# Kernel tuning notes

Hardware: AMD Instinct MI355X
Metric: run time of the kernel (lower is better)

The kernel has to match this reference:

```python
import jax, jax.numpy as jnp
import numpy as np

N, C, H, O, NUM_CLASSES = 4096, 768, 512, 50, 1


def setup_inputs() -> dict:
    key = jax.random.key(0)
    ks = jax.random.split(key, 8)
    x = jax.random.normal(ks[0], (N, C), dtype=jnp.float32)
    labels = jax.random.randint(ks[1], (N,), 0, 2, dtype=jnp.int64)
    W1 = jax.random.normal(ks[2], (C, H), dtype=jnp.float32) / np.sqrt(C)
    b1 = jnp.zeros((H,), dtype=jnp.float32)
    W2 = jax.random.normal(ks[3], (H, O), dtype=jnp.float32) / np.sqrt(H)
    b2 = jnp.zeros((O,), dtype=jnp.float32)
    fcW = jax.random.normal(ks[4], (C + O, NUM_CLASSES), dtype=jnp.float32) / np.sqrt(C + O)
    fcb = jnp.zeros((NUM_CLASSES,), dtype=jnp.float32)
    return {"x": x, "labels": labels, "W1": W1, "b1": b1, "W2": W2, "b2": b2, "fcW": fcW, "fcb": fcb}


def _build_graph(x, labels):
    # similarity-threshold edge construction (dense masked form of the python double loop)
    sim = x @ x.T                                   # [N, N]
    n = x.shape[0]
    diff = labels[:, None] != labels[None, :]       # cross-label pairs
    cnt = jnp.sum(diff)
    s = jnp.sum(jnp.where(diff, sim, 0.0))
    threshold = jnp.where(cnt > 0, s / cnt.astype(sim.dtype), jnp.asarray(0.0, sim.dtype))
    eye = jnp.eye(n, dtype=bool)
    same = (labels[:, None] == labels[None, :]) & ~eye
    edge_mask = same & (sim <= threshold)           # symmetric (sim symmetric)
    loss_mask = edge_mask & (jnp.arange(n)[:, None] < jnp.arange(n)[None, :])  # i<j pairs
    adj = jax.lax.stop_gradient(edge_mask.astype(x.dtype))
    # GCN normalization with self-loops
    a = adj + jnp.eye(n, dtype=x.dtype)
    dinv = jax.lax.rsqrt(jnp.sum(a, axis=1))        # deg >= 1
    norm_adj = dinv[:, None] * a * dinv[None, :]
    return norm_adj, loss_mask


def reference(x, labels, W1, b1, W2, b2, fcW, fcb):
    norm_adj, loss_mask = _build_graph(x, labels)
    h = jax.nn.relu(norm_adj @ (x @ W1) + b1)       # conv1 + relu
    g = norm_adj @ (h @ W2) + b2                    # conv2
    f_g = jnp.concatenate([x, g], axis=-1)          # [N, C+O]
    out = f_g @ fcW + fcb                           # [N, 1]
    return out, f_g, loss_mask, x
```

## Files before the change

kernel.cpp:

```cpp
#include <hip/hip_runtime.h>
#include <hip/hip_bf16.h>
#include <math.h>

#define NN 4096
#define CD 768
#define HD 512
#define OD 50
#define FGD 818

typedef short short8 __attribute__((ext_vector_type(8)));
typedef _Float16 half8 __attribute__((ext_vector_type(8)));
typedef float f32x4 __attribute__((ext_vector_type(4)));
typedef unsigned short us4 __attribute__((ext_vector_type(4)));
typedef unsigned short ushortT;
typedef unsigned char uchar;
typedef unsigned long long u64;

__device__ inline ushortT f2bf(float v) {
    __hip_bfloat16 b = __float2bfloat16(v);
    return *(ushortT*)&b;
}
__device__ inline float bf2f(ushortT u) {
    __hip_bfloat16 b = *(__hip_bfloat16*)&u;
    return __bfloat162float(b);
}
__device__ inline float dinv_of(int d) {
    return (float)(1.0 / sqrt((double)(1 + d)));
}

__global__ __launch_bounds__(256) void gsum_kernel(const float* __restrict__ x,
                                                   const int* __restrict__ labels,
                                                   double* __restrict__ gsum) {
    int b = blockIdx.x;
    int t = threadIdx.x;
    double a0[3] = {0, 0, 0}, a1[3] = {0, 0, 0};
    for (int rr = 0; rr < 16; ++rr) {
        int row = b * 16 + rr;
        int lab = labels[row];
#pragma unroll
        for (int s = 0; s < 3; ++s) {
            double v = (double)x[(size_t)row * CD + t + s * 256];
            if (lab == 0) a0[s] += v; else a1[s] += v;
        }
    }
#pragma unroll
    for (int s = 0; s < 3; ++s) {
        atomicAdd(&gsum[t + s * 256], a0[s]);
        atomicAdd(&gsum[768 + t + s * 256], a1[s]);
    }
}

__global__ __launch_bounds__(256) void gdot_kernel(const double* __restrict__ gsum,
                                                   const int* __restrict__ labels,
                                                   double* __restrict__ scal) {
    int t = threadIdx.x;
    double d = 0.0;
    for (int c = t; c < CD; c += 256) d += gsum[c] * gsum[768 + c];
    int n0 = 0;
    for (int i = t; i < NN; i += 256) n0 += (labels[i] == 0) ? 1 : 0;
    for (int off = 32; off; off >>= 1) {
        d += __shfl_down(d, off);
        n0 += __shfl_down(n0, off);
    }
    __shared__ double sd[4];
    __shared__ int sn[4];
    int wid = t >> 6, lane = t & 63;
    if (lane == 0) { sd[wid] = d; sn[wid] = n0; }
    __syncthreads();
    if (t == 0) {
        double D = sd[0] + sd[1] + sd[2] + sd[3];
        double N0 = (double)(sn[0] + sn[1] + sn[2] + sn[3]);
        scal[0] = 2.0 * D;
        scal[1] = 2.0 * N0 * ((double)NN - N0);
    }
}

#define BAND 0.10
#define RC_CAP (1 << 18)
#define RCB 256

__global__ __launch_bounds__(256) void sim_fused(
    const ushortT* __restrict__ xf, const int* __restrict__ labels,
    const double* __restrict__ scal, u64* __restrict__ abbits,
    float* __restrict__ lm, int* __restrict__ deg,
    int* __restrict__ rc_cnt, int* __restrict__ rc_list) {
    int bid = blockIdx.x;
    int sid = (bid & 7) * 260 + (bid >> 3);
    int sby = 0, rem = sid;
    for (; sby < 8; ++sby) {
        int rowsz = 36 + (7 - sby) * 64;
        if (rem < rowsz) break;
        rem -= rowsz;
    }
    int sbx, iby, ibx;
    if (rem < 36) {
        sbx = sby;
        iby = 0;
        while (rem >= 8 - iby) { rem -= 8 - iby; ++iby; }
        ibx = iby + rem;
    } else {
        rem -= 36;
        sbx = sby + 1 + (rem >> 6);
        int u = rem & 63;
        iby = u >> 3; ibx = u & 7;
    }
    int by = sby * 8 + iby, bx = sbx * 8 + ibx;
    bool diag = (bx == by);

    __shared__ ushortT lds[2 * 64 * 72];
    __shared__ int larr[128];
    __shared__ int rcbuf[RCB];
    __shared__ int rcn, rcbase;
    int tid = threadIdx.x;
    int lane = tid & 63;
    int w = tid >> 6;
    int wr = w >> 1, wc = w & 1;
    int m = lane & 15, quad = lane >> 4;
    int row0 = by * 64, col0 = bx * 64;

    if (tid == 0) rcn = 0;
    if (tid < 64) larr[tid] = labels[row0 + tid];
    else if (tid < 128) larr[tid] = labels[col0 + tid - 64];

    f32x4 acc[2][2] = {{{0.f, 0.f, 0.f, 0.f}, {0.f, 0.f, 0.f, 0.f}},
                       {{0.f, 0.f, 0.f, 0.f}, {0.f, 0.f, 0.f, 0.f}}};

    const size_t rowbase = (size_t)row0 * CD;
    const size_t colbase = (size_t)col0 * CD;
    short8 rg[2][2];
#pragma unroll
    for (int tt = 0; tt < 2; ++tt) {
        int id2 = tid + tt * 256;
        int row = id2 >> 3, c8 = (id2 & 7) * 8;
        rg[tt][0] = *(const short8*)&xf[rowbase + (size_t)row * CD + c8];
        rg[tt][1] = *(const short8*)&xf[colbase + (size_t)row * CD + c8];
    }

    for (int k0 = 0; k0 < CD; k0 += 64) {
        __syncthreads();
#pragma unroll
        for (int tt = 0; tt < 2; ++tt) {
            int id2 = tid + tt * 256;
            int row = id2 >> 3, c8 = (id2 & 7) * 8;
            *(short8*)&lds[0 * 4608 + row * 72 + c8] = rg[tt][0];
            *(short8*)&lds[1 * 4608 + row * 72 + c8] = rg[tt][1];
        }
        __syncthreads();
        if (k0 + 64 < CD) {
#pragma unroll
            for (int tt = 0; tt < 2; ++tt) {
                int id2 = tid + tt * 256;
                int row = id2 >> 3, c8 = (id2 & 7) * 8 + k0 + 64;
                rg[tt][0] = *(const short8*)&xf[rowbase + (size_t)row * CD + c8];
                rg[tt][1] = *(const short8*)&xf[colbase + (size_t)row * CD + c8];
            }
        }
#pragma unroll
        for (int ks = 0; ks < 2; ++ks) {
            half8 ah[2], bh[2];
#pragma unroll
            for (int i = 0; i < 2; ++i)
                ah[i] = *(const half8*)&lds[(wr * 32 + i * 16 + m) * 72 +
                                            ks * 32 + quad * 8];
#pragma unroll
            for (int j = 0; j < 2; ++j)
                bh[j] = *(const half8*)&lds[4608 + (wc * 32 + j * 16 + m) * 72 +
                                            ks * 32 + quad * 8];
#pragma unroll
            for (int i = 0; i < 2; ++i)
#pragma unroll
                for (int j = 0; j < 2; ++j)
                    acc[i][j] = __builtin_amdgcn_mfma_f32_16x16x32_f16(
                        ah[i], bh[j], acc[i][j], 0, 0, 0);
        }
    }
    __syncthreads();

    double thrd;
    {
        double cnt = scal[1];
        thrd = (cnt > 0.0) ? (scal[0] / cnt) : 0.0;
    }
    uchar* flags = (uchar*)lds;
#pragma unroll
    for (int i = 0; i < 2; ++i)
#pragma unroll
        for (int j = 0; j < 2; ++j) {
#pragma unroll
            for (int r = 0; r < 4; ++r) {
                int row = wr * 32 + i * 16 + quad * 4 + r;
                int col = wc * 32 + j * 16 + m;
                bool same = (larr[row] == larr[64 + col]);
                bool selfp = ((row0 + row) == (col0 + col));
                bool edge = false;
                if (same && !selfp) {
                    double s = (double)acc[i][j][r];
                    if (s <= thrd - BAND) {
                        edge = true;
                    } else if (s <= thrd + BAND) {
                        edge = (s <= thrd);
                        int enc = ((row0 + row) << 12) | (col0 + col) |
                                  (diag ? 0 : (1 << 24)) |
                                  (edge ? (1 << 25) : 0);
                        int slot = atomicAdd(&rcn, 1);
                        if (slot < RCB) rcbuf[slot] = enc;
                    }
                }
                flags[row * 68 + col] = edge ? 1 : 0;
            }
        }
    __syncthreads();
    if (tid == 0) {
        int n = rcn < RCB ? rcn : RCB;
        rcbase = n ? atomicAdd(rc_cnt, n) : 0;
    }

    {
        int r = tid >> 2, q = tid & 3;
        int cnti = 0;
        unsigned int bits16 = 0;
#pragma unroll
        for (int s = 0; s < 4; ++s) {
            int cb = q * 16 + s * 4;
            float4 f;
#pragma unroll
            for (int k2 = 0; k2 < 4; ++k2) {
                int c = cb + k2;
                bool fl = flags[r * 68 + c] != 0;
                cnti += fl ? 1 : 0;
                if (fl || (diag && r == c)) bits16 |= 1u << (s * 4 + k2);
                ((float*)&f)[k2] = (fl && (row0 + r < col0 + c)) ? 1.0f : 0.0f;
            }
            *(float4*)&lm[(size_t)(row0 + r) * NN + col0 + cb] = f;
        }
        unsigned int s1 = __shfl_down(bits16, 1);
        unsigned int s2 = __shfl_down(bits16, 2);
        unsigned int s3 = __shfl_down(bits16, 3);
        cnti += __shfl_down(cnti, 1);
        cnti += __shfl_down(cnti, 2);
        if (q == 0) {
            u64 u = (u64)bits16 | ((u64)s1 << 16) | ((u64)s2 << 32) |
                    ((u64)s3 << 48);
            abbits[(size_t)(row0 + r) * 64 + bx] = u;
            if (cnti) atomicAdd(&deg[row0 + r], cnti);
        }
    }

    if (!diag) {
        int c = tid >> 2, q = tid & 3;
        int cnti = 0;
        unsigned int bits16 = 0;
        float4 fz = {0.0f, 0.0f, 0.0f, 0.0f};
#pragma unroll
        for (int s = 0; s < 4; ++s) {
            int rb = q * 16 + s * 4;
#pragma unroll
            for (int k2 = 0; k2 < 4; ++k2) {
                bool fl = flags[(rb + k2) * 68 + c] != 0;
                cnti += fl ? 1 : 0;
                if (fl) bits16 |= 1u << (s * 4 + k2);
            }
            *(float4*)&lm[(size_t)(col0 + c) * NN + row0 + rb] = fz;
        }
        unsigned int s1 = __shfl_down(bits16, 1);
        unsigned int s2 = __shfl_down(bits16, 2);
        unsigned int s3 = __shfl_down(bits16, 3);
        cnti += __shfl_down(cnti, 1);
        cnti += __shfl_down(cnti, 2);
        if (q == 0) {
            u64 u = (u64)bits16 | ((u64)s1 << 16) | ((u64)s2 << 32) |
                    ((u64)s3 << 48);
            abbits[(size_t)(col0 + c) * 64 + by] = u;
            if (cnti) atomicAdd(&deg[col0 + c], cnti);
        }
    }

    __syncthreads();
    {
        int n = rcn < RCB ? rcn : RCB;
        if (tid < n) {
            int idx = rcbase + tid;
            if (idx < RC_CAP) rc_list[idx] = rcbuf[tid];
        }
    }
}

__global__ __launch_bounds__(256) void rc_fix(
    const float* __restrict__ x, const double* __restrict__ scal,
    const int* __restrict__ rc_cnt, const int* __restrict__ rc_list,
    u64* __restrict__ abbits, float* __restrict__ lm, int* __restrict__ deg) {
    int cnt = *rc_cnt;
    if (cnt > RC_CAP) cnt = RC_CAP;
    double thrd;
    {
        double c = scal[1];
        thrd = (c > 0.0) ? (scal[0] / c) : 0.0;
    }
    int lane = threadIdx.x & 63;
    int wid = (blockIdx.x * 256 + threadIdx.x) >> 6;
    int nw = (gridDim.x * 256) >> 6;
    for (int e = wid; e < cnt; e += nw) {
        int enc = rc_list[e];
        int c = enc & 0xFFF;
        int r = (enc >> 12) & 0xFFF;
        bool mirror = (enc >> 24) & 1;
        bool prov = (enc >> 25) & 1;
        const float* xi = x + (size_t)r * CD;
        const float* xj = x + (size_t)c * CD;
        double d = 0.0;
#pragma unroll
        for (int s = 0; s < 12; ++s)
            d += (double)xi[lane + s * 64] * (double)xj[lane + s * 64];
        for (int off = 32; off; off >>= 1) d += __shfl_down(d, off);
        if (lane == 0) {
            bool exact = (d <= thrd);
            if (exact != prov) {
                u64 mk = 1ull << (c & 63);
                if (exact) atomicOr(&abbits[(size_t)r * 64 + (c >> 6)], mk);
                else       atomicAnd(&abbits[(size_t)r * 64 + (c >> 6)], ~mk);
                lm[(size_t)r * NN + c] = (exact && r < c) ? 1.0f : 0.0f;
                int dlt = exact ? 1 : -1;
                atomicAdd(&deg[r], dlt);
                if (mirror) {
                    u64 mk2 = 1ull << (r & 63);
                    if (exact) atomicOr(&abbits[(size_t)c * 64 + (r >> 6)], mk2);
                    else       atomicAnd(&abbits[(size_t)c * 64 + (r >> 6)], ~mk2);
                    atomicAdd(&deg[c], dlt);
                }
            }
        }
    }
}

__global__ __launch_bounds__(256) void prep_kernel(
    const float* __restrict__ x, const float* __restrict__ W1,
    const float* __restrict__ W2, float* __restrict__ fg, float* __restrict__ xo,
    ushortT* __restrict__ xh, ushortT* __restrict__ xf, ushortT* __restrict__ w1t,
    ushortT* __restrict__ w2t) {
    int b = blockIdx.x;
    if (b < 4096) {
        int t = threadIdx.x;
        if (t < 192) {
            float4 v = *(const float4*)&x[(size_t)b * CD + t * 4];
            *(float4*)&xo[(size_t)b * CD + t * 4] = v;
            fg[(size_t)b * FGD + t * 4 + 0] = v.x;
            fg[(size_t)b * FGD + t * 4 + 1] = v.y;
            fg[(size_t)b * FGD + t * 4 + 2] = v.z;
            fg[(size_t)b * FGD + t * 4 + 3] = v.w;
            us4 hh, ff;
            float* vp = (float*)&v;
#pragma unroll
            for (int k = 0; k < 4; ++k) {
                ((ushortT*)&hh)[k] = f2bf(vp[k]);
                _Float16 g = (_Float16)vp[k];
                ((ushortT*)&ff)[k] = *(ushortT*)&g;
            }
            *(us4*)&xh[(size_t)b * CD + t * 4] = hh;
            *(us4*)&xf[(size_t)b * CD + t * 4] = ff;
        }
        return;
    }
    __shared__ float tT[32][33];
    const float* P;
    ushortT* T;
    int K, N, Npad, k0, n0;
    if (b < 4480) {
        int bb = b - 4096;
        P = W1; T = w1t; K = CD; N = HD; Npad = HD;
        k0 = (bb % 24) * 32; n0 = (bb / 24) * 32;
    } else {
        int bb = b - 4480;
        P = W2; T = w2t; K = HD; N = OD; Npad = 64;
        k0 = (bb % 16) * 32; n0 = (bb / 16) * 32;
    }
    int tx = threadIdx.x & 31, ty = threadIdx.x >> 5;
#pragma unroll
    for (int s = 0; s < 4; ++s) {
        int k = k0 + ty + s * 8, n = n0 + tx;
        tT[ty + s * 8][tx] = (k < K && n < N) ? P[(size_t)k * N + n] : 0.0f;
    }
    __syncthreads();
#pragma unroll
    for (int s = 0; s < 4; ++s) {
        int n = n0 + ty + s * 8, k = k0 + tx;
        if (n < Npad && k < K) T[(size_t)n * K + k] = f2bf(tT[tx][ty + s * 8]);
    }
}

template <bool RELU, bool HASBIAS, int EPI>
__global__ __launch_bounds__(256) void gemm_bf16(
    const ushortT* __restrict__ A, const ushortT* __restrict__ B,
    ushortT* __restrict__ Cb, int M, int Nn, int K, int ldc,
    const int* __restrict__ deg, const float* __restrict__ bias) {
    __shared__ ushortT lds[2 * 64 * 72];
    int tid = threadIdx.x;
    int lane = tid & 63;
    int w = tid >> 6;
    int wr = w >> 1, wc = w & 1;
    int m = lane & 15, quad = lane >> 4;
    int row0 = blockIdx.y * 64, col0 = blockIdx.x * 64;

    f32x4 acc[2][2] = {{{0.f, 0.f, 0.f, 0.f}, {0.f, 0.f, 0.f, 0.f}},
                       {{0.f, 0.f, 0.f, 0.f}, {0.f, 0.f, 0.f, 0.f}}};

    for (int k0 = 0; k0 < K; k0 += 64) {
#pragma unroll
        for (int t = 0; t < 2; ++t) {
            int id2 = tid + t * 256;
            int row = id2 >> 3, c8 = (id2 & 7) * 8;
            *(short8*)&lds[row * 72 + c8] =
                *(const short8*)&A[(size_t)(row0 + row) * K + k0 + c8];
            *(short8*)&lds[4608 + row * 72 + c8] =
                *(const short8*)&B[(size_t)(col0 + row) * K + k0 + c8];
        }
        __syncthreads();
#pragma unroll
        for (int ks = 0; ks < 2; ++ks) {
            short8 af[2], bf[2];
#pragma unroll
            for (int i = 0; i < 2; ++i)
                af[i] = *(const short8*)&lds[(wr * 32 + i * 16 + m) * 72 +
                                             ks * 32 + quad * 8];
#pragma unroll
            for (int j = 0; j < 2; ++j)
                bf[j] = *(const short8*)&lds[4608 + (wc * 32 + j * 16 + m) * 72 +
                                             ks * 32 + quad * 8];
#pragma unroll
            for (int i = 0; i < 2; ++i)
#pragma unroll
                for (int j = 0; j < 2; ++j)
                    acc[i][j] = __builtin_amdgcn_mfma_f32_16x16x32_bf16(
                        af[i], bf[j], acc[i][j], 0, 0, 0);
        }
        __syncthreads();
    }

    if (EPI == 2) {
        ushortT* Th = lds;
#pragma unroll
        for (int i = 0; i < 2; ++i)
#pragma unroll
            for (int j = 0; j < 2; ++j)
#pragma unroll
                for (int r = 0; r < 4; ++r) {
                    int row = wr * 32 + i * 16 + quad * 4 + r;
                    int col = wc * 32 + j * 16 + m;
                    float dv = dinv_of(deg[row0 + row]);
                    Th[col * 72 + row] = f2bf(acc[i][j][r] * dv);
                }
        __syncthreads();
#pragma unroll
        for (int t = 0; t < 2; ++t) {
            int id2 = tid + t * 256;
            int cc = id2 >> 3, chunk = id2 & 7;
            *(short8*)&Cb[(size_t)(col0 + cc) * M + row0 + chunk * 8] =
                *(const short8*)&Th[cc * 72 + chunk * 8];
        }
    } else {
#pragma unroll
        for (int i = 0; i < 2; ++i)
#pragma unroll
            for (int j = 0; j < 2; ++j)
#pragma unroll
                for (int r = 0; r < 4; ++r) {
                    int row = wr * 32 + i * 16 + quad * 4 + r;
                    int col = wc * 32 + j * 16 + m;
                    int gr = row0 + row, gc = col0 + col;
                    if (gc < Nn) {
                        float v = acc[i][j][r] * dinv_of(deg[gr]);
                        if (HASBIAS) v += bias[gc];
                        if (RELU) v = fmaxf(v, 0.0f);
                        Cb[(size_t)gr * ldc + gc] = f2bf(v);
                    }
                }
    }
}

__global__ __launch_bounds__(256) void gemm_part(
    const ushortT* __restrict__ A, const ushortT* __restrict__ B,
    float* __restrict__ P, int M, int K, int KC) {
    __shared__ ushortT lds[2 * 64 * 72];
    int tid = threadIdx.x;
    int lane = tid & 63;
    int w = tid >> 6;
    int wr = w >> 1, wc = w & 1;
    int m = lane & 15, quad = lane >> 4;
    int kb = blockIdx.x;
    int row0 = blockIdx.y * 64;
    int kbase = kb * KC;

    f32x4 acc[2][2] = {{{0.f, 0.f, 0.f, 0.f}, {0.f, 0.f, 0.f, 0.f}},
                       {{0.f, 0.f, 0.f, 0.f}, {0.f, 0.f, 0.f, 0.f}}};

    for (int k0 = 0; k0 < KC; k0 += 64) {
#pragma unroll
        for (int t = 0; t < 2; ++t) {
            int id2 = tid + t * 256;
            int row = id2 >> 3, c8 = (id2 & 7) * 8;
            *(short8*)&lds[row * 72 + c8] =
                *(const short8*)&A[(size_t)(row0 + row) * K + kbase + k0 + c8];
            *(short8*)&lds[4608 + row * 72 + c8] =
                *(const short8*)&B[(size_t)row * K + kbase + k0 + c8];
        }
        __syncthreads();
#pragma unroll
        for (int ks = 0; ks < 2; ++ks) {
            short8 af[2], bf[2];
#pragma unroll
            for (int i = 0; i < 2; ++i)
                af[i] = *(const short8*)&lds[(wr * 32 + i * 16 + m) * 72 +
                                             ks * 32 + quad * 8];
#pragma unroll
            for (int j = 0; j < 2; ++j)
                bf[j] = *(const short8*)&lds[4608 + (wc * 32 + j * 16 + m) * 72 +
                                             ks * 32 + quad * 8];
#pragma unroll
            for (int i = 0; i < 2; ++i)
#pragma unroll
                for (int j = 0; j < 2; ++j)
                    acc[i][j] = __builtin_amdgcn_mfma_f32_16x16x32_bf16(
                        af[i], bf[j], acc[i][j], 0, 0, 0);
        }
        __syncthreads();
    }
#pragma unroll
    for (int i = 0; i < 2; ++i)
#pragma unroll
        for (int j = 0; j < 2; ++j)
#pragma unroll
            for (int r = 0; r < 4; ++r) {
                int row = wr * 32 + i * 16 + quad * 4 + r;
                int col = wc * 32 + j * 16 + m;
                P[((size_t)kb * M + row0 + row) * 64 + col] = acc[i][j][r];
            }
}

__global__ __launch_bounds__(256) void gemm_partB(
    const u64* __restrict__ Abits, const ushortT* __restrict__ B,
    float* __restrict__ P, int M, int K, int KC) {
    __shared__ ushortT lds[2 * 64 * 72];
    int tid = threadIdx.x;
    int lane = tid & 63;
    int w = tid >> 6;
    int wr = w >> 1, wc = w & 1;
    int m = lane & 15, quad = lane >> 4;
    int kb = blockIdx.x;
    int row0 = blockIdx.y * 64;
    int kbase = kb * KC;
    int er = tid >> 2, eq = tid & 3;

    f32x4 acc[2][2] = {{{0.f, 0.f, 0.f, 0.f}, {0.f, 0.f, 0.f, 0.f}},
                       {{0.f, 0.f, 0.f, 0.f}, {0.f, 0.f, 0.f, 0.f}}};

    for (int k0 = 0; k0 < KC; k0 += 64) {
#pragma unroll
        for (int t = 0; t < 2; ++t) {
            int id2 = tid + t * 256;
            int row = id2 >> 3, c8 = (id2 & 7) * 8;
            *(short8*)&lds[4608 + row * 72 + c8] =
                *(const short8*)&B[(size_t)row * K + kbase + k0 + c8];
        }
        {
            u64 bits = Abits[(size_t)(row0 + er) * 64 + ((kbase + k0) >> 6)];
            unsigned int half = (unsigned int)(bits >> (eq * 16)) & 0xFFFFu;
            short8 v0, v1;
#pragma unroll
            for (int k = 0; k < 8; ++k) {
                ((ushortT*)&v0)[k] =
                    ((half >> k) & 1) ? (ushortT)0x3F80 : (ushortT)0;
                ((ushortT*)&v1)[k] =
                    ((half >> (k + 8)) & 1) ? (ushortT)0x3F80 : (ushortT)0;
            }
            *(short8*)&lds[er * 72 + eq * 16] = v0;
            *(short8*)&lds[er * 72 + eq * 16 + 8] = v1;
        }
        __syncthreads();
#pragma unroll
        for (int ks = 0; ks < 2; ++ks) {
            short8 af[2], bf[2];
#pragma unroll
            for (int i = 0; i < 2; ++i)
                af[i] = *(const short8*)&lds[(wr * 32 + i * 16 + m) * 72 +
                                             ks * 32 + quad * 8];
#pragma unroll
            for (int j = 0; j < 2; ++j)
                bf[j] = *(const short8*)&lds[4608 + (wc * 32 + j * 16 + m) * 72 +
                                             ks * 32 + quad * 8];
#pragma unroll
            for (int i = 0; i < 2; ++i)
#pragma unroll
                for (int j = 0; j < 2; ++j)
                    acc[i][j] = __builtin_amdgcn_mfma_f32_16x16x32_bf16(
                        af[i], bf[j], acc[i][j], 0, 0, 0);
        }
        __syncthreads();
    }
#pragma unroll
    for (int i = 0; i < 2; ++i)
#pragma unroll
        for (int j = 0; j < 2; ++j)
#pragma unroll
            for (int r = 0; r < 4; ++r) {
                int row = wr * 32 + i * 16 + quad * 4 + r;
                int col = wc * 32 + j * 16 + m;
                P[((size_t)kb * M + row0 + row) * 64 + col] = acc[i][j][r];
            }
}

__global__ __launch_bounds__(256) void gemm_partWB(
    const u64* __restrict__ Abits, const ushortT* __restrict__ B,
    float* __restrict__ P, int M, int K, int KC, int ldP) {
    __shared__ ushortT lds[2 * 64 * 72];
    int tid = threadIdx.x;
    int lane = tid & 63;
    int w = tid >> 6;
    int wr = w >> 1, wc = w & 1;
    int m = lane & 15, quad = lane >> 4;
    int col0 = blockIdx.x * 64;
    int row0 = blockIdx.y * 64;
    int kb = blockIdx.z;
    int kbase = kb * KC;
    int er = tid >> 2, eq = tid & 3;

    f32x4 acc[2][2] = {{{0.f, 0.f, 0.f, 0.f}, {0.f, 0.f, 0.f, 0.f}},
                       {{0.f, 0.f, 0.f, 0.f}, {0.f, 0.f, 0.f, 0.f}}};

    for (int k0 = 0; k0 < KC; k0 += 64) {
#pragma unroll
        for (int t = 0; t < 2; ++t) {
            int id2 = tid + t * 256;
            int row = id2 >> 3, c8 = (id2 & 7) * 8;
            *(short8*)&lds[4608 + row * 72 + c8] =
                *(const short8*)&B[(size_t)(col0 + row) * K + kbase + k0 + c8];
        }
        {
            u64 bits = Abits[(size_t)(row0 + er) * 64 + ((kbase + k0) >> 6)];
            unsigned int half = (unsigned int)(bits >> (eq * 16)) & 0xFFFFu;
            short8 v0, v1;
#pragma unroll
            for (int k = 0; k < 8; ++k) {
                ((ushortT*)&v0)[k] =
                    ((half >> k) & 1) ? (ushortT)0x3F80 : (ushortT)0;
                ((ushortT*)&v1)[k] =
                    ((half >> (k + 8)) & 1) ? (ushortT)0x3F80 : (ushortT)0;
            }
            *(short8*)&lds[er * 72 + eq * 16] = v0;
            *(short8*)&lds[er * 72 + eq * 16 + 8] = v1;
        }
        __syncthreads();
#pragma unroll
        for (int ks = 0; ks < 2; ++ks) {
            short8 af[2], bf[2];
#pragma unroll
            for (int i = 0; i < 2; ++i)
                af[i] = *(const short8*)&lds[(wr * 32 + i * 16 + m) * 72 +
                                             ks * 32 + quad * 8];
#pragma unroll
            for (int j = 0; j < 2; ++j)
                bf[j] = *(const short8*)&lds[4608 + (wc * 32 + j * 16 + m) * 72 +
                                             ks * 32 + quad * 8];
#pragma unroll
            for (int i = 0; i < 2; ++i)
#pragma unroll
                for (int j = 0; j < 2; ++j)
                    acc[i][j] = __builtin_amdgcn_mfma_f32_16x16x32_bf16(
                        af[i], bf[j], acc[i][j], 0, 0, 0);
        }
        __syncthreads();
    }
#pragma unroll
    for (int i = 0; i < 2; ++i)
#pragma unroll
        for (int j = 0; j < 2; ++j)
#pragma unroll
            for (int r = 0; r < 4; ++r) {
                int row = wr * 32 + i * 16 + quad * 4 + r;
                int col = wc * 32 + j * 16 + m;
                P[((size_t)kb * M + row0 + row) * ldP + col0 + col] =
                    acc[i][j][r];
            }
}

__global__ __launch_bounds__(256) void k5_epi(const float* __restrict__ P5,
                                              const int* __restrict__ deg,
                                              const float* __restrict__ b1,
                                              ushortT* __restrict__ hb) {
    int tid = threadIdx.x;
    int cg = tid & 127;
    int rr = tid >> 7;
#pragma unroll
    for (int p = 0; p < 2; ++p) {
        int r = blockIdx.x * 4 + p * 2 + rr;
        float dv = dinv_of(deg[r]);
        float4 s = {0.f, 0.f, 0.f, 0.f};
#pragma unroll
        for (int kb = 0; kb < 4; ++kb) {
            float4 v = *(const float4*)&P5[((size_t)kb * NN + r) * HD + cg * 4];
            s.x += v.x; s.y += v.y; s.z += v.z; s.w += v.w;
        }
        float4 bv = *(const float4*)&b1[cg * 4];
        us4 o;
        o[0] = f2bf(fmaxf(s.x * dv + bv.x, 0.f));
        o[1] = f2bf(fmaxf(s.y * dv + bv.y, 0.f));
        o[2] = f2bf(fmaxf(s.z * dv + bv.z, 0.f));
        o[3] = f2bf(fmaxf(s.w * dv + bv.w, 0.f));
        *(us4*)&hb[(size_t)r * HD + cg * 4] = o;
    }
}

__global__ __launch_bounds__(256) void k6_epi(const float* __restrict__ P6,
                                              const int* __restrict__ deg,
                                              ushortT* __restrict__ hw2sT) {
    __shared__ ushortT Th[64 * 72];
    int row0 = blockIdx.x * 64;
    int tid = threadIdx.x;
    int rl = tid >> 2, q = tid & 3;
    float dv = dinv_of(deg[row0 + rl]);
#pragma unroll
    for (int s = 0; s < 16; ++s) {
        int c = q * 16 + s;
        float v = 0.f;
#pragma unroll
        for (int kb = 0; kb < 8; ++kb)
            v += P6[((size_t)kb * NN + row0 + rl) * 64 + c];
        Th[c * 72 + rl] = f2bf(v * dv);
    }
    __syncthreads();
#pragma unroll
    for (int t = 0; t < 2; ++t) {
        int id2 = tid + t * 256;
        int cc = id2 >> 3, chunk = id2 & 7;
        *(short8*)&hw2sT[(size_t)cc * NN + row0 + chunk * 8] =
            *(const short8*)&Th[cc * 72 + chunk * 8];
    }
}

__global__ __launch_bounds__(256) void k7_epi_out(
    const float* __restrict__ P7, const int* __restrict__ deg,
    const float* __restrict__ b2, const float* __restrict__ fcW,
    const float* __restrict__ fcb, float* __restrict__ fg,
    float* __restrict__ out) {
    int row0 = blockIdx.x * 64;
    int tid = threadIdx.x;
    int rl = tid >> 2, q = tid & 3;
    int r = row0 + rl;
    float dv = dinv_of(deg[r]);
    float sg = 0.f;
#pragma unroll
    for (int s = 0; s < 16; ++s) {
        int c = q * 16 + s;
        if (c < OD) {
            float v = 0.f;
#pragma unroll
            for (int kb = 0; kb < 16; ++kb)
                v += P7[((size_t)kb * NN + r) * 64 + c];
            v = v * dv + b2[c];
            fg[(size_t)r * FGD + CD + c] = v;
            sg += v * fcW[CD + c];
        }
    }
    const float* fr = fg + (size_t)r * FGD;
    float sx = 0.f;
    for (int k = q * 192; k < (q + 1) * 192; k += 2) {
        float2 vv = *(const float2*)&fr[k];
        float2 ww = *(const float2*)&fcW[k];
        sx += vv.x * ww.x + vv.y * ww.y;
    }
    float s = sx + sg;
    s += __shfl_down(s, 1);
    s += __shfl_down(s, 2);
    if (q == 0) out[r] = s + fcb[0];
}

extern "C" void kernel_launch(void* const* d_in, const int* in_sizes, int n_in,
                              void* d_out, int out_size, void* d_ws, size_t ws_size,
                              hipStream_t stream) {
    const float* x = (const float*)d_in[0];
    const int* labels = (const int*)d_in[1];
    const float* W1 = (const float*)d_in[2];
    const float* b1 = (const float*)d_in[3];
    const float* W2 = (const float*)d_in[4];
    const float* b2 = (const float*)d_in[5];
    const float* fcW = (const float*)d_in[6];
    const float* fcb = (const float*)d_in[7];
    float* outp = (float*)d_out;

    const size_t o_out = 0;
    const size_t o_fg = 4096;
    const size_t o_lm = o_fg + (size_t)NN * FGD;
    const size_t o_x = o_lm + (size_t)NN * NN;

    char* ws = (char*)d_ws;
    size_t off = 0;
    u64* abbits = (u64*)(ws + off); off += (size_t)NN * 64 * 8;
    ushortT* xh = (ushortT*)(ws + off); off += (size_t)NN * CD * 2;
    ushortT* xf = (ushortT*)(ws + off); off += (size_t)NN * CD * 2;
    ushortT* w1t = (ushortT*)(ws + off); off += (size_t)HD * CD * 2;
    ushortT* xw1sT = (ushortT*)(ws + off); off += (size_t)HD * NN * 2;
    ushortT* hb = (ushortT*)(ws + off); off += (size_t)NN * HD * 2;
    ushortT* w2t = (ushortT*)(ws + off); off += (size_t)64 * HD * 2;
    ushortT* hw2sT = (ushortT*)(ws + off); off += (size_t)64 * NN * 2;
    char* zbase = ws + off;
    int* deg = (int*)(ws + off); off += (size_t)NN * 4;
    double* gsum = (double*)(ws + off); off += 1536 * 8;
    double* scal = (double*)(ws + off); off += 16;
    int* rc_cnt = (int*)(ws + off); off += 16;
    size_t zbytes = (size_t)NN * 4 + 1536 * 8 + 16 + 16;
    char* uni = ws + off;
    int* rc_list = (int*)uni;
    float* P5 = (float*)uni;
    float* P6 = (float*)uni;
    float* P7 = (float*)uni;
    off += (size_t)4 * NN * HD * 4;

    hipMemsetAsync(zbase, 0, zbytes, stream);

    prep_kernel<<<4512, 256, 0, stream>>>(x, W1, W2, outp + o_fg, outp + o_x, xh, xf,
                                          w1t, w2t);

    gsum_kernel<<<256, 256, 0, stream>>>(x, labels, gsum);
    gdot_kernel<<<1, 256, 0, stream>>>(gsum, labels, scal);

    sim_fused<<<2080, 256, 0, stream>>>(xf, labels, scal, abbits, outp + o_lm,
                                        deg, rc_cnt, rc_list);

    rc_fix<<<512, 256, 0, stream>>>(x, scal, rc_cnt, rc_list, abbits, outp + o_lm,
                                    deg);

    gemm_bf16<false, false, 2><<<dim3(HD / 64, NN / 64), 256, 0, stream>>>(
        xh, w1t, xw1sT, NN, HD, CD, 0, deg, nullptr);

    gemm_partWB<<<dim3(HD / 64, NN / 64, 4), 256, 0, stream>>>(
        abbits, xw1sT, P5, NN, NN, NN / 4, HD);
    k5_epi<<<NN / 4, 256, 0, stream>>>(P5, deg, b1, hb);

    gemm_part<<<dim3(8, NN / 64), 256, 0, stream>>>(hb, w2t, P6, NN, HD, HD / 8);
    k6_epi<<<NN / 64, 256, 0, stream>>>(P6, deg, hw2sT);

    gemm_partB<<<dim3(16, NN / 64), 256, 0, stream>>>(abbits, hw2sT, P7, NN, NN,
                                                      NN / 16);
    k7_epi_out<<<NN / 64, 256, 0, stream>>>(P7, deg, b2, fcW, fcb, outp + o_fg,
                                            outp + o_out);
}
```

Measured before the change: 325.0 us.

## Fuse gsum into prep and X·W1 GEMM into sim kernel grid

Folds the per-label column-sum kernel into extra blocks of the prep kernel, and moves the X·W1 GEMM into extra blocks of the similarity kernel so it runs concurrently, writing unscaled fp32 transposed output. A new elementwise kernel then applies the degree normalization and converts to bf16, since degrees are only final after rc_fix. This cuts launches and fills the tail of the similarity grid, at the cost of an extra fp32 round trip through global memory (8 MB) and a separate scaling pass.

```diff
diff --git a/kernel.cpp b/kernel.cpp
--- a/kernel.cpp
+++ b/kernel.cpp
@@ -26,28 +26,6 @@
 }
 __device__ inline float dinv_of(int d) {
     return (float)(1.0 / sqrt((double)(1 + d)));
-}
-
-__global__ __launch_bounds__(256) void gsum_kernel(const float* __restrict__ x,
-                                                   const int* __restrict__ labels,
-                                                   double* __restrict__ gsum) {
-    int b = blockIdx.x;
-    int t = threadIdx.x;
-    double a0[3] = {0, 0, 0}, a1[3] = {0, 0, 0};
-    for (int rr = 0; rr < 16; ++rr) {
-        int row = b * 16 + rr;
-        int lab = labels[row];
-#pragma unroll
-        for (int s = 0; s < 3; ++s) {
-            double v = (double)x[(size_t)row * CD + t + s * 256];
-            if (lab == 0) a0[s] += v; else a1[s] += v;
-        }
-    }
-#pragma unroll
-    for (int s = 0; s < 3; ++s) {
-        atomicAdd(&gsum[t + s * 256], a0[s]);
-        atomicAdd(&gsum[768 + t + s * 256], a1[s]);
-    }
 }
 
 __global__ __launch_bounds__(256) void gdot_kernel(const double* __restrict__ gsum,
@@ -79,11 +57,71 @@
 #define RC_CAP (1 << 18)
 #define RCB 256
 
-__global__ __launch_bounds__(256) void sim_fused(
-    const ushortT* __restrict__ xf, const int* __restrict__ labels,
+__global__ __launch_bounds__(256) void simk4(
+    const ushortT* __restrict__ xf, const ushortT* __restrict__ xh,
+    const ushortT* __restrict__ w1t, const int* __restrict__ labels,
     const double* __restrict__ scal, u64* __restrict__ abbits,
     float* __restrict__ lm, int* __restrict__ deg,
-    int* __restrict__ rc_cnt, int* __restrict__ rc_list) {
+    int* __restrict__ rc_cnt, int* __restrict__ rc_list,
+    float* __restrict__ xw1f) {
+    __shared__ ushortT lds[2 * 64 * 72];
+    __shared__ int larr[128];
+    __shared__ int rcbuf[RCB];
+    __shared__ int rcn, rcbase;
+    int tid = threadIdx.x;
+    int lane = tid & 63;
+    int w = tid >> 6;
+    int wr = w >> 1, wc = w & 1;
+    int m = lane & 15, quad = lane >> 4;
+
+    if (blockIdx.x >= 2080) {
+        int idx = blockIdx.x - 2080;
+        int row0 = (idx >> 3) * 64, col0 = (idx & 7) * 64;
+        f32x4 acc[2][2] = {{{0.f, 0.f, 0.f, 0.f}, {0.f, 0.f, 0.f, 0.f}},
+                           {{0.f, 0.f, 0.f, 0.f}, {0.f, 0.f, 0.f, 0.f}}};
+        for (int k0 = 0; k0 < CD; k0 += 64) {
+#pragma unroll
+            for (int t = 0; t < 2; ++t) {
+                int id2 = tid + t * 256;
+                int row = id2 >> 3, c8 = (id2 & 7) * 8;
+                *(short8*)&lds[row * 72 + c8] =
+                    *(const short8*)&xh[(size_t)(row0 + row) * CD + k0 + c8];
+                *(short8*)&lds[4608 + row * 72 + c8] =
+                    *(const short8*)&w1t[(size_t)(col0 + row) * CD + k0 + c8];
+            }
+            __syncthreads();
+#pragma unroll
+            for (int ks = 0; ks < 2; ++ks) {
+                short8 af[2], bf[2];
+#pragma unroll
+                for (int i = 0; i < 2; ++i)
+                    af[i] = *(const short8*)&lds[(wr * 32 + i * 16 + m) * 72 +
+                                                 ks * 32 + quad * 8];
+#pragma unroll
+                for (int j = 0; j < 2; ++j)
+                    bf[j] = *(const short8*)&lds[4608 +
+                                                 (wc * 32 + j * 16 + m) * 72 +
+                                                 ks * 32 + quad * 8];
+#pragma unroll
+                for (int i = 0; i < 2; ++i)
+#pragma unroll
+                    for (int j = 0; j < 2; ++j)
+                        acc[i][j] = __builtin_amdgcn_mfma_f32_16x16x32_bf16(
+                            af[i], bf[j], acc[i][j], 0, 0, 0);
+            }
+            __syncthreads();
+        }
+#pragma unroll
+        for (int i = 0; i < 2; ++i)
+#pragma unroll
+            for (int j = 0; j < 2; ++j) {
+                int row = row0 + wr * 32 + i * 16 + quad * 4;
+                int col = col0 + wc * 32 + j * 16 + m;
+                *(f32x4*)&xw1f[(size_t)col * NN + row] = acc[i][j];
+            }
+        return;
+    }
+
     int bid = blockIdx.x;
     int sid = (bid & 7) * 260 + (bid >> 3);
     int sby = 0, rem = sid;
@@ -106,16 +144,6 @@
     }
     int by = sby * 8 + iby, bx = sbx * 8 + ibx;
     bool diag = (bx == by);
-
-    __shared__ ushortT lds[2 * 64 * 72];
-    __shared__ int larr[128];
-    __shared__ int rcbuf[RCB];
-    __shared__ int rcn, rcbase;
-    int tid = threadIdx.x;
-    int lane = tid & 63;
-    int w = tid >> 6;
-    int wr = w >> 1, wc = w & 1;
-    int m = lane & 15, quad = lane >> 4;
     int row0 = by * 64, col0 = bx * 64;
 
     if (tid == 0) rcn = 0;
@@ -332,11 +360,26 @@
     }
 }
 
+__global__ __launch_bounds__(256) void scaleT(const float* __restrict__ xw1f,
+                                              const int* __restrict__ deg,
+                                              ushortT* __restrict__ xw1sT) {
+    size_t i = ((size_t)blockIdx.x * 256 + threadIdx.x) * 4;
+    float4 v = *(const float4*)&xw1f[i];
+    int r = (int)(i & (NN - 1));
+    us4 o;
+    o[0] = f2bf(v.x / sqrtf((float)(1 + deg[r])));
+    o[1] = f2bf(v.y / sqrtf((float)(1 + deg[r + 1])));
+    o[2] = f2bf(v.z / sqrtf((float)(1 + deg[r + 2])));
+    o[3] = f2bf(v.w / sqrtf((float)(1 + deg[r + 3])));
+    *(us4*)&xw1sT[i] = o;
+}
+
 __global__ __launch_bounds__(256) void prep_kernel(
     const float* __restrict__ x, const float* __restrict__ W1,
-    const float* __restrict__ W2, float* __restrict__ fg, float* __restrict__ xo,
+    const float* __restrict__ W2, const int* __restrict__ labels,
+    float* __restrict__ fg, float* __restrict__ xo,
     ushortT* __restrict__ xh, ushortT* __restrict__ xf, ushortT* __restrict__ w1t,
-    ushortT* __restrict__ w2t) {
+    ushortT* __restrict__ w2t, double* __restrict__ gsum) {
     int b = blockIdx.x;
     if (b < 4096) {
         int t = threadIdx.x;
@@ -360,6 +403,26 @@
         }
         return;
     }
+    if (b >= 4512) {
+        int bb = b - 4512;
+        int t = threadIdx.x;
+        double a0[3] = {0, 0, 0}, a1[3] = {0, 0, 0};
+        for (int rr = 0; rr < 16; ++rr) {
+            int row = bb * 16 + rr;
+            int lab = labels[row];
+#pragma unroll
+            for (int s = 0; s < 3; ++s) {
+                double v = (double)x[(size_t)row * CD + t + s * 256];
+                if (lab == 0) a0[s] += v; else a1[s] += v;
+            }
+        }
+#pragma unroll
+        for (int s = 0; s < 3; ++s) {
+            atomicAdd(&gsum[t + s * 256], a0[s]);
+            atomicAdd(&gsum[768 + t + s * 256], a1[s]);
+        }
+        return;
+    }
     __shared__ float tT[32][33];
     const float* P;
     ushortT* T;
@@ -384,95 +447,6 @@
     for (int s = 0; s < 4; ++s) {
         int n = n0 + ty + s * 8, k = k0 + tx;
         if (n < Npad && k < K) T[(size_t)n * K + k] = f2bf(tT[tx][ty + s * 8]);
-    }
-}
-
-template <bool RELU, bool HASBIAS, int EPI>
-__global__ __launch_bounds__(256) void gemm_bf16(
-    const ushortT* __restrict__ A, const ushortT* __restrict__ B,
-    ushortT* __restrict__ Cb, int M, int Nn, int K, int ldc,
-    const int* __restrict__ deg, const float* __restrict__ bias) {
-    __shared__ ushortT lds[2 * 64 * 72];
-    int tid = threadIdx.x;
-    int lane = tid & 63;
-    int w = tid >> 6;
-    int wr = w >> 1, wc = w & 1;
-    int m = lane & 15, quad = lane >> 4;
-    int row0 = blockIdx.y * 64, col0 = blockIdx.x * 64;
-
-    f32x4 acc[2][2] = {{{0.f, 0.f, 0.f, 0.f}, {0.f, 0.f, 0.f, 0.f}},
-                       {{0.f, 0.f, 0.f, 0.f}, {0.f, 0.f, 0.f, 0.f}}};
-
-    for (int k0 = 0; k0 < K; k0 += 64) {
-#pragma unroll
-        for (int t = 0; t < 2; ++t) {
-            int id2 = tid + t * 256;
-            int row = id2 >> 3, c8 = (id2 & 7) * 8;
-            *(short8*)&lds[row * 72 + c8] =
-                *(const short8*)&A[(size_t)(row0 + row) * K + k0 + c8];
-            *(short8*)&lds[4608 + row * 72 + c8] =
-                *(const short8*)&B[(size_t)(col0 + row) * K + k0 + c8];
-        }
-        __syncthreads();
-#pragma unroll
-        for (int ks = 0; ks < 2; ++ks) {
-            short8 af[2], bf[2];
-#pragma unroll
-            for (int i = 0; i < 2; ++i)
-                af[i] = *(const short8*)&lds[(wr * 32 + i * 16 + m) * 72 +
-                                             ks * 32 + quad * 8];
-#pragma unroll
-            for (int j = 0; j < 2; ++j)
-                bf[j] = *(const short8*)&lds[4608 + (wc * 32 + j * 16 + m) * 72 +
-                                             ks * 32 + quad * 8];
-#pragma unroll
-            for (int i = 0; i < 2; ++i)
-#pragma unroll
-                for (int j = 0; j < 2; ++j)
-                    acc[i][j] = __builtin_amdgcn_mfma_f32_16x16x32_bf16(
-                        af[i], bf[j], acc[i][j], 0, 0, 0);
-        }
-        __syncthreads();
-    }
-
-    if (EPI == 2) {
-        ushortT* Th = lds;
-#pragma unroll
-        for (int i = 0; i < 2; ++i)
-#pragma unroll
-            for (int j = 0; j < 2; ++j)
-#pragma unroll
-                for (int r = 0; r < 4; ++r) {
-                    int row = wr * 32 + i * 16 + quad * 4 + r;
-                    int col = wc * 32 + j * 16 + m;
-                    float dv = dinv_of(deg[row0 + row]);
-                    Th[col * 72 + row] = f2bf(acc[i][j][r] * dv);
-                }
-        __syncthreads();
-#pragma unroll
-        for (int t = 0; t < 2; ++t) {
-            int id2 = tid + t * 256;
-            int cc = id2 >> 3, chunk = id2 & 7;
-            *(short8*)&Cb[(size_t)(col0 + cc) * M + row0 + chunk * 8] =
-                *(const short8*)&Th[cc * 72 + chunk * 8];
-        }
-    } else {
-#pragma unroll
-        for (int i = 0; i < 2; ++i)
-#pragma unroll
-            for (int j = 0; j < 2; ++j)
-#pragma unroll
-                for (int r = 0; r < 4; ++r) {
-                    int row = wr * 32 + i * 16 + quad * 4 + r;
-                    int col = wc * 32 + j * 16 + m;
-                    int gr = row0 + row, gc = col0 + col;
-                    if (gc < Nn) {
-                        float v = acc[i][j][r] * dinv_of(deg[gr]);
-                        if (HASBIAS) v += bias[gc];
-                        if (RELU) v = fmaxf(v, 0.0f);
-                        Cb[(size_t)gr * ldc + gc] = f2bf(v);
-                    }
-                }
     }
 }
 
@@ -808,6 +782,7 @@
     size_t zbytes = (size_t)NN * 4 + 1536 * 8 + 16 + 16;
     char* uni = ws + off;
     int* rc_list = (int*)uni;
+    float* xw1f = (float*)(uni + (1 << 20));
     float* P5 = (float*)uni;
     float* P6 = (float*)uni;
     float* P7 = (float*)uni;
@@ -815,20 +790,18 @@
 
     hipMemsetAsync(zbase, 0, zbytes, stream);
 
-    prep_kernel<<<4512, 256, 0, stream>>>(x, W1, W2, outp + o_fg, outp + o_x, xh, xf,
-                                          w1t, w2t);
-
-    gsum_kernel<<<256, 256, 0, stream>>>(x, labels, gsum);
+    prep_kernel<<<4768, 256, 0, stream>>>(x, W1, W2, labels, outp + o_fg,
+                                          outp + o_x, xh, xf, w1t, w2t, gsum);
+
     gdot_kernel<<<1, 256, 0, stream>>>(gsum, labels, scal);
 
-    sim_fused<<<2080, 256, 0, stream>>>(xf, labels, scal, abbits, outp + o_lm,
-                                        deg, rc_cnt, rc_list);
+    simk4<<<2592, 256, 0, stream>>>(xf, xh, w1t, labels, scal, abbits,
+                                    outp + o_lm, deg, rc_cnt, rc_list, xw1f);
 
     rc_fix<<<512, 256, 0, stream>>>(x, scal, rc_cnt, rc_list, abbits, outp + o_lm,
                                     deg);
 
-    gemm_bf16<false, false, 2><<<dim3(HD / 64, NN / 64), 256, 0, stream>>>(
-        xh, w1t, xw1sT, NN, HD, CD, 0, deg, nullptr);
+    scaleT<<<(HD * NN / 4) / 256, 256, 0, stream>>>(xw1f, deg, xw1sT);
 
     gemm_partWB<<<dim3(HD / 64, NN / 64, 4), 256, 0, stream>>>(
         abbits, xw1sT, P5, NN, NN, NN / 4, HD);
```

Result: faster. 306.8 us (-5.6%).
